# Performance work log

Measured on AMD Instinct MI355X. Metric: run time of the kernel, lower is better.

The kernel has to match this reference:

```python
import jax, jax.numpy as jnp
import numpy as np

CM = 8        # channel_mult
EPS = 1e-5    # BatchNorm eps
NEG = 0.2     # LeakyReLU slope


def conv2d(x, w, stride, pad, b=None):
    y = jax.lax.conv_general_dilated(
        x, w, (stride, stride), [(pad, pad), (pad, pad)],
        dimension_numbers=('NCHW', 'OIHW', 'NCHW'))
    if b is not None:
        y = y + b[None, :, None, None]
    return y


def per_sample_conv(x, w, stride, pad):
    # x: [B,C,H,W], w: [B,O,C,kh,kw] -> per-sample conv, vmapped over batch
    f = lambda xi, wi: conv2d(xi[None], wi, stride, pad)[0]
    return jax.vmap(f)(x, w)


def batchnorm(x, g, b):
    # training-mode BN: batch statistics over (N,H,W)
    m = jnp.mean(x, axis=(0, 2, 3), keepdims=True)
    v = jnp.var(x, axis=(0, 2, 3), keepdims=True)
    return (x - m) * jax.lax.rsqrt(v + EPS) * g[None, :, None, None] + b[None, :, None, None]


def lrelu(x):
    return jnp.where(x >= 0, x, NEG * x)


def setup_inputs() -> dict:
    key = jax.random.key(0)
    ks = jax.random.split(key, 16)
    B, H, W = 16, 512, 512

    def rn(k, shape, fan_in):
        return jax.random.normal(k, shape, jnp.float32) * np.float32(1.0 / np.sqrt(fan_in))

    inp = {}
    inp['x'] = jax.random.normal(ks[0], (B, 3, H, W), jnp.float32)
    n_meta = 3 * (CM // 2) * 25 + CM * (CM * 2 // 2) * 25  # 300 + 1600 = 1900
    inp['conv_weights'] = jax.random.normal(ks[1], (B, n_meta), jnp.float32) * 0.05
    inp['w11'] = rn(ks[2], (CM // 2, 3, 5, 5), 3 * 25)
    inp['b11'] = jnp.zeros((CM // 2,), jnp.float32)
    inp['w12'] = rn(ks[3], (CM * 2 // 2, CM, 5, 5), CM * 25)
    inp['b12'] = jnp.zeros((CM * 2 // 2,), jnp.float32)
    inp['bn1_g'] = jnp.ones((CM * 2,), jnp.float32)
    inp['bn1_b'] = jnp.zeros((CM * 2,), jnp.float32)
    # conv2 stack: (in, out, kernel)
    chans = [(CM * 2, CM * 4, 5), (CM * 4, CM * 8, 5), (CM * 8, CM * 16, 3), (CM * 16, CM * 16, 3)]
    for i, (ci, co, k) in enumerate(chans, 1):
        inp[f'c2w{i}'] = rn(ks[3 + i], (co, ci, k, k), ci * k * k)
        inp[f'c2b{i}'] = jnp.zeros((co,), jnp.float32)
        inp[f'bn{i}g'] = jnp.ones((co,), jnp.float32)
        inp[f'bn{i}b'] = jnp.zeros((co,), jnp.float32)
    return inp


def reference(x, conv_weights, w11, b11, w12, b12, bn1_g, bn1_b,
              c2w1, c2b1, bn1g, bn1b, c2w2, c2b2, bn2g, bn2b,
              c2w3, c2b3, bn3g, bn3b, c2w4, c2b4, bn4g, bn4b):
    B, _, H, W = x.shape
    n1 = 3 * (CM // 2) * 25
    w1 = conv_weights[:, :n1].reshape(B, CM // 2, 3, 5, 5)
    w2 = conv_weights[:, n1:].reshape(B, CM * 2 // 2, CM, 5, 5)

    # meta layer 1: shared half + per-sample dynamic half
    xx = conv2d(x, w11, 1, 2, b11)                  # [B, cm/2, H, W]
    half = per_sample_conv(x, w1, 1, 2)             # [B, cm/2, H, W]
    h = lrelu(jnp.concatenate([xx, half], axis=1))  # [B, cm, H, W]

    # meta layer 2 (stride 2)
    xx = conv2d(h, w12, 2, 2, b12)                  # [B, cm, H/2, W/2]
    half = per_sample_conv(h, w2, 2, 2)             # [B, cm, H/2, W/2]
    h = lrelu(batchnorm(jnp.concatenate([xx, half], axis=1), bn1_g, bn1_b))

    # dense conv stack
    for w_, b_, g_, be_, p in [
        (c2w1, c2b1, bn1g, bn1b, 2),
        (c2w2, c2b2, bn2g, bn2b, 2),
        (c2w3, c2b3, bn3g, bn3b, 1),
        (c2w4, c2b4, bn4g, bn4b, 1),
    ]:
        h = lrelu(batchnorm(conv2d(h, w_, 2, p, b_), g_, be_))

    return h.reshape(-1, CM * 16, H // 32, W // 32)
```

## Files before the change

kernel.cpp:

```cpp
#include <hip/hip_runtime.h>


typedef __attribute__((ext_vector_type(8))) short short8v;
typedef __attribute__((ext_vector_type(4))) float float4v;
typedef __attribute__((ext_vector_type(4))) unsigned short ushort4v;
typedef unsigned short u16;

#define LRELU_NEG 0.2f
#define BN_EPS 1e-5f

__device__ __forceinline__ float bf2f(u16 u){ union{unsigned i; float f;} v; v.i=(unsigned)u<<16; return v.f; }
__device__ __forceinline__ u16 f2bf(float f){ unsigned x=__float_as_uint(f); x += 0x7FFFu + ((x>>16)&1u); return (u16)(x>>16); }
__device__ __forceinline__ float lrelu(float v){ return v<0.f? LRELU_NEG*v : v; }

__device__ __forceinline__ void packw(int i, const float* __restrict__ w, u16* __restrict__ dst,
                                      int IC, int OC, int KSZ, int CPR) {
  int kq = i & 31, oc = (i>>5) % OC, c = i/(OC*32);
  int ky = c / CPR, r = c % CPR;
  int kk = r*32 + kq; int kx = kk / IC, ic = kk % IC;
  float v = (kx < KSZ) ? w[(((size_t)oc*IC + ic)*KSZ + ky)*KSZ + kx] : 0.f;
  dst[i] = f2bf(v);
}

__global__ __launch_bounds__(256) void prep_all(
    const float* __restrict__ w11, const float* __restrict__ w12,
    const float* __restrict__ b12, const float* __restrict__ cw,
    const float* __restrict__ wc1, const float* __restrict__ wc2,
    const float* __restrict__ wc3, const float* __restrict__ wc4,
    u16* __restrict__ wl1d, u16* __restrict__ wl2m, float* __restrict__ bl2,
    u16* __restrict__ d1, u16* __restrict__ d2, u16* __restrict__ d3, u16* __restrict__ d4,
    u16* __restrict__ h1) {
  int i = blockIdx.x*256 + threadIdx.x;
  if (i < 16) {
    bl2[i] = (i<8)? b12[i] : 0.f;
  } else if (i < 49168) {
    int j = i - 16;
    int b = j / 3072, r = j % 3072;
    int c = r >> 9, r2 = r & 511;
    int row = r2 >> 5, kk = r2 & 31;
    int kx = kk >> 2, ic = kk & 3;
    int grp = row >> 3, oc = row & 7;
    int ky = c - grp;
    float v = 0.f;
    if (ic < 3 && kx < 5 && ky >= 0 && ky < 5)
      v = (oc < 4) ? w11[((oc*3+ic)*5+ky)*5+kx]
                   : cw[b*1900 + (oc-4)*75 + ic*25 + ky*5 + kx];
    wl1d[j] = f2bf(v);
  } else if (i < 131088) {
    int j = i - 49168;
    int kq = j & 31, oc = (j>>5) & 15, c = (j>>9) % 10, b = j / 5120;
    int ky = c >> 1, r = c & 1;
    int kk = r*32 + kq; int kx = kk >> 3, ic = kk & 7;
    float v = 0.f;
    if (kx < 5)
      v = (oc < 8) ? w12[((oc*8+ic)*5+ky)*5+kx]
                   : cw[b*1900 + 300 + ((oc-8)*8+ic)*25 + ky*5 + kx];
    wl2m[j] = f2bf(v);
  } else if (i < 196880) {
    int j = i - 131088;
    int b = j / 4112, p = j % 4112;
    int y, xx;
    if (p < 2064) { int r = p/516; y = (r<2)? r : 512+r; xx = p%516; }
    else          { int q = p-2064; int cidx = q&3; xx = (cidx<2)? cidx : 512+cidx; y = 2 + (q>>2); }
    short8v z = {0,0,0,0,0,0,0,0};
    *(short8v*)(h1 + (((size_t)b*516 + y)*516 + xx)*8) = z;
  } else if (i < 484624) {
    int j = i - 196880;
    if (j < 15360) packw(j, wc1, d1, 16, 32, 5, 3);
    else if (j < 66560) packw(j-15360, wc2, d2, 32, 64, 5, 5);
    else if (j < 140288) packw(j-66560, wc3, d3, 64, 128, 3, 6);
    else packw(j-140288, wc4, d4, 128, 128, 3, 12);
  }
}

__global__ __launch_bounds__(256) void conv_l1(const float* __restrict__ x,
    const u16* __restrict__ wl1d, const float* __restrict__ b11,
    u16* __restrict__ h1) {
  __shared__ __align__(16) u16 sx[20*72*4 + 32];
  const int tid = threadIdx.x, b = blockIdx.z;
  const int x0 = (blockIdx.x & 7) * 64;
  const int r0 = (blockIdx.x >> 3) * 16;

  if (tid < 32) sx[20*72*4 + tid] = 0;

  const bool interior = (r0 >= 16) & (r0 <= 480) & (x0 >= 64) & (x0 <= 384);
  if (interior) {
    for (int e = tid; e < 360; e += 256) {
      int row = e / 18, cg = e % 18;
      size_t base = ((size_t)b*3*512 + r0 + row - 2)*512 + x0 + cg*4 - 4;
      float4v p0 = *(const float4v*)(x + base);
      float4v p1 = *(const float4v*)(x + base + 262144);
      float4v p2 = *(const float4v*)(x + base + 524288);
      short8v lo, hi;
#pragma unroll
      for (int j = 0; j < 2; j++) {
        lo[4*j+0] = (short)f2bf(p0[j]);   lo[4*j+1] = (short)f2bf(p1[j]);
        lo[4*j+2] = (short)f2bf(p2[j]);   lo[4*j+3] = 0;
        hi[4*j+0] = (short)f2bf(p0[j+2]); hi[4*j+1] = (short)f2bf(p1[j+2]);
        hi[4*j+2] = (short)f2bf(p2[j+2]); hi[4*j+3] = 0;
      }
      u16* dp = sx + (row*72 + cg*4)*4;
      *(short8v*)dp = lo;
      *(short8v*)(dp + 8) = hi;
    }
  } else {
    for (int e = tid; e < 1440; e += 256) {
      int row = e / 72, col = e % 72;
      int gy = r0 + row - 2, gx = x0 + col - 4;
      float v0 = 0.f, v1 = 0.f, v2 = 0.f;
      if (gy >= 0 && gy < 512 && gx >= 0 && gx < 512) {
        size_t base = ((size_t)b*3*512 + gy)*512 + gx;
        v0 = x[base]; v1 = x[base + 262144]; v2 = x[base + 524288];
      }
      ushort4 pk = {f2bf(v0), f2bf(v1), f2bf(v2), 0};
      *(ushort4*)(sx + e*4) = pk;
    }
  }
  __syncthreads();

  const int lane = tid & 63, w = tid >> 6;
  const int l15 = lane & 15, sub = lane >> 4;

  short8v Wf[6];
  const u16* wb = wl1d + (size_t)b*3072;
#pragma unroll
  for (int c = 0; c < 6; c++)
    Wf[c] = *(const short8v*)(wb + (c*16 + l15)*32 + sub*8);

  float bvv[4];
#pragma unroll
  for (int r = 0; r < 4; r++) bvv[r] = (sub & 1) ? 0.f : b11[r];

  const int colb = w*16 + l15;
  const int oc0 = (sub & 1) * 4;
  const int rsel = sub >> 1;

#pragma unroll
  for (int p = 0; p < 8; p++) {
    float4v acc = {0.f, 0.f, 0.f, 0.f};
#pragma unroll
    for (int c = 0; c < 6; c++) {
      const u16* ap = sx + (((2*p + c)*72 + colb + 2) << 2) + sub*8;
      union { unsigned long long q[2]; short8v v; } ua;
      ua.q[0] = *(const unsigned long long*)(ap);
      ua.q[1] = *(const unsigned long long*)(ap + 4);
      acc = __builtin_amdgcn_mfma_f32_16x16x32_bf16(Wf[c], ua.v, acc, 0, 0, 0);
    }
    ushort4v pk;
#pragma unroll
    for (int r = 0; r < 4; r++) pk[r] = f2bf(lrelu(acc[r] + bvv[r]));
    int outrow = r0 + 2*p + rsel;
    u16* dst = h1 + (((size_t)b*516 + outrow + 2)*516 + x0 + colb + 2)*8 + oc0;
    *(ushort4v*)dst = pk;
  }
}

#define LOADC(cc, Ax, Bx) do {                                                   \
    const int ky_ = (cc) / CPR, r_ = (cc) % CPR;                                 \
    const int kk0_ = r_*32 + sub*8;                                              \
    const int kx_ = kk0_ / IC, ico_ = kk0_ % IC;                                 \
    _Pragma("unroll") for (int n_ = 0; n_ < WN; n_++)                            \
      Bx[n_] = *(const short8v*)(wbase + ((size_t)(cc)*OC + oc0 + n_*16 + l15)*32 + sub*8); \
    _Pragma("unroll") for (int f_ = 0; f_ < WM; f_++) {                          \
      int iy_ = S*oyf[f_] + ky_ + PADOFF;                                        \
      Ax[f_] = *(const short8v*)(inb + ((size_t)iy_*IPW + ixb[f_] + kx_)*IC + ico_); \
    }                                                                            \
  } while(0)

#define MFMAC(Ax, Bx) do {                                                       \
    _Pragma("unroll") for (int f_ = 0; f_ < WM; f_++)                            \
      _Pragma("unroll") for (int n_ = 0; n_ < WN; n_++)                          \
        acc[f_][n_] = __builtin_amdgcn_mfma_f32_16x16x32_bf16(Ax[f_], Bx[n_], acc[f_][n_], 0, 0, 0); \
  } while(0)

template <int IC, int OC, int KSZ, int S, int P, int CPR, int NCH,
          int IPH, int IPW, int OWL, int OPH, int OPW,
          int WM, int WN, int WVM, int WVN, bool PERS>
__global__ __launch_bounds__(WVM*WVN*64) void conv_mfma(
    const u16* __restrict__ in, const u16* __restrict__ wmfma,
    const float* __restrict__ bias, u16* __restrict__ out,
    float2* __restrict__ part2) {
  constexpr int OW = 1 << OWL;
  constexpr int PADOFF = 2 - P;
  const int tid = threadIdx.x, lane = tid & 63;
  const int w = tid >> 6, wm = w % WVM, wn = w / WVM;
  const int l15 = lane & 15, sub = lane >> 4;
  const int b = blockIdx.z;
  const int px0 = blockIdx.x * (16*WM*WVM) + wm * (16*WM);
  const int oc0 = blockIdx.y * (16*WN*WVN) + wn * (16*WN);

  int oyf[WM], oxb[WM], ixb[WM];
#pragma unroll
  for (int f = 0; f < WM; f++) {
    int p = px0 + f*16;
    oyf[f] = p >> OWL;
    oxb[f] = p & (OW-1);
    ixb[f] = S*(oxb[f] + l15) + PADOFF;
  }
  const u16* inb = in + (size_t)b*IPH*IPW*IC;
  const u16* wbase = wmfma + (PERS ? (size_t)b*NCH*OC*32 : (size_t)0);

  float4v acc[WM][WN];
#pragma unroll
  for (int f = 0; f < WM; f++)
#pragma unroll
    for (int n = 0; n < WN; n++) acc[f][n] = (float4v){0.f,0.f,0.f,0.f};

  constexpr int NC = KSZ * CPR;
  short8v A0[WM], B0[WN], A1[WM], B1[WN];
  LOADC(0, A0, B0);
#pragma unroll
  for (int c = 0; c < NC; c += 2) {
    if (c + 1 < NC) LOADC(c + 1, A1, B1);
    MFMAC(A0, B0);
    if (c + 2 < NC) LOADC(c + 2, A0, B0);
    if (c + 1 < NC) MFMAC(A1, B1);
  }

  float s[WN], q[WN];
#pragma unroll
  for (int n = 0; n < WN; n++) { s[n] = 0.f; q[n] = 0.f; }
#pragma unroll
  for (int f = 0; f < WM; f++) {
    const int oxs = oxb[f] + sub*4;
    const size_t rowb = ((size_t)b*OPH + oyf[f] + 2)*OPW;
#pragma unroll
    for (int n = 0; n < WN; n++) {
      int oc = oc0 + n*16 + l15;
      float bv = bias[oc];
#pragma unroll
      for (int rr = 0; rr < 4; rr++) {
        float v = acc[f][n][rr] + bv;
        out[(rowb + oxs + rr + 2)*OC + oc] = f2bf(v);
        s[n] += v; q[n] += v*v;
      }
    }
  }
#pragma unroll
  for (int n = 0; n < WN; n++) {
    s[n] += __shfl_xor(s[n], 16); s[n] += __shfl_xor(s[n], 32);
    q[n] += __shfl_xor(q[n], 16); q[n] += __shfl_xor(q[n], 32);
  }
  __shared__ float sred[WVM*WVN][WN][16][2];
  if (sub == 0) {
#pragma unroll
    for (int n = 0; n < WN; n++) { sred[w][n][l15][0] = s[n]; sred[w][n][l15][1] = q[n]; }
  }
  __syncthreads();
  const int NBp = gridDim.x * gridDim.z;
  const int pb = blockIdx.z * gridDim.x + blockIdx.x;
  const int tot = WVN*WN*16;
  if (tid < tot) {
    int c16 = tid & 15, n = (tid >> 4) % WN, wn2 = tid / (16*WN);
    float S_ = 0.f, Q_ = 0.f;
    for (int wm2 = 0; wm2 < WVM; wm2++) {
      S_ += sred[wn2*WVM + wm2][n][c16][0];
      Q_ += sred[wn2*WVM + wm2][n][c16][1];
    }
    int c = blockIdx.y*(16*WN*WVN) + wn2*(16*WN) + n*16 + c16;
    part2[(size_t)c*NBp + pb] = make_float2(S_, Q_);
  }
}

__global__ void bn_stage2(const float2* __restrict__ part2, const float* __restrict__ g,
                          const float* __restrict__ bb, float* __restrict__ stats,
                          int NBp, float invN) {
  int c = blockIdx.x;
  float s = 0.f, q = 0.f;
  for (int i = threadIdx.x; i < NBp; i += 64) {
    float2 p = part2[(size_t)c*NBp + i];
    s += p.x; q += p.y;
  }
  for (int o = 32; o > 0; o >>= 1) { s += __shfl_down(s, o); q += __shfl_down(q, o); }
  if (threadIdx.x == 0) {
    float m = s * invN;
    float var = q * invN - m*m;
    float sc = g[c] * rsqrtf(var + BN_EPS);
    stats[2*c] = sc;
    stats[2*c+1] = bb[c] - m*sc;
  }
}

template <int C, int PH, int PW, int HH, int WW>
__global__ __launch_bounds__(256) void bn_fin(u16* __restrict__ y, const float* __restrict__ stats,
                                              int total8) {
  int i = blockIdx.x*256 + threadIdx.x;
  if (i >= total8) return;
  size_t e = (size_t)i*8;
  int c0 = (int)(e & (C-1));
  int px = (int)(e / C);
  int xx = px % PW;
  int yy = (px / PW) % PH;
  bool interior = (yy >= 2) & (yy < 2+HH) & (xx >= 2) & (xx < 2+WW);
  short8v u = *(short8v*)(y + e);
  short8v o;
#pragma unroll
  for (int j = 0; j < 8; j++) {
    float v = bf2f((u16)u[j]) * stats[2*(c0+j)] + stats[2*(c0+j)+1];
    o[j] = interior ? (short)f2bf(lrelu(v)) : (short)0;
  }
  *(short8v*)(y + e) = o;
}

__global__ __launch_bounds__(256) void out_k(const u16* __restrict__ y6,
                                             const float* __restrict__ stats,
                                             float* __restrict__ out) {
  int i = blockIdx.x*256 + threadIdx.x;
  if (i >= 131072) return;
  size_t e = (size_t)i*4;
  int c0 = (int)(e & 127);
  int px = (int)(e >> 7);
  int loc = px & 255, b = px >> 8;
  int y = loc >> 4, x = loc & 15;
  const u16* src = y6 + (((size_t)b*20 + y + 2)*20 + x + 2)*128 + c0;
  ushort4 u = *(const ushort4*)src;
  float vv[4] = {bf2f(u.x), bf2f(u.y), bf2f(u.z), bf2f(u.w)};
#pragma unroll
  for (int j = 0; j < 4; j++) {
    int c = c0 + j;
    float v = vv[j] * stats[2*c] + stats[2*c+1];
    out[(((size_t)b*128 + c) << 8) + loc] = lrelu(v);
  }
}

extern "C" void kernel_launch(void* const* d_in, const int* in_sizes, int n_in,
                              void* d_out, int out_size, void* d_ws, size_t ws_size,
                              hipStream_t stream) {
  const float* x    = (const float*)d_in[0];
  const float* cw   = (const float*)d_in[1];
  const float* w11  = (const float*)d_in[2];
  const float* b11  = (const float*)d_in[3];
  const float* w12  = (const float*)d_in[4];
  const float* b12  = (const float*)d_in[5];
  const float* bn1g = (const float*)d_in[6];
  const float* bn1b = (const float*)d_in[7];
  const float* c2w[4] = {(const float*)d_in[8], (const float*)d_in[12],
                         (const float*)d_in[16], (const float*)d_in[20]};
  const float* c2b[4] = {(const float*)d_in[9], (const float*)d_in[13],
                         (const float*)d_in[17], (const float*)d_in[21]};
  const float* bng[4] = {(const float*)d_in[10], (const float*)d_in[14],
                         (const float*)d_in[18], (const float*)d_in[22]};
  const float* bnb[4] = {(const float*)d_in[11], (const float*)d_in[15],
                         (const float*)d_in[19], (const float*)d_in[23]};

  char* ws = (char*)d_ws;
  u16* h1   = (u16*)(ws);
  u16* y3   = (u16*)(ws);
  u16* y4   = (u16*)(ws + 17842176);
  u16* y5   = (u16*)(ws + 27312128);
  u16* y6   = (u16*)(ws + 32620544);
  u16* yT2  = (u16*)(ws + 68158464);
  u16* wl2m = (u16*)(ws + 102769664);
  float* bl2    = (float*)(ws + 102933504);
  float2* part2 = (float2*)(ws + 102933568);
  float* stats2 = (float*)(ws + 103457856);
  float* stats3 = stats2 + 32;
  float* stats4 = stats3 + 64;
  float* stats5 = stats4 + 128;
  float* stats6 = stats5 + 256;
  u16* wl1d = (u16*)(ws + 103460800);
  u16* wS1  = (u16*)(ws + 103559104);
  u16* wS2  = (u16*)(ws + 103589824);
  u16* wS3  = (u16*)(ws + 103692224);
  u16* wS4  = (u16*)(ws + 103839680);

  prep_all<<<1894, 256, 0, stream>>>(w11, w12, b12, cw,
                                     c2w[0], c2w[1], c2w[2], c2w[3],
                                     wl1d, wl2m, bl2, wS1, wS2, wS3, wS4, h1);

  conv_l1<<<dim3(256, 1, 16), 256, 0, stream>>>(x, wl1d, b11, h1);

  conv_mfma<8,16,5,2,2, 2,10, 516,516, 8, 260,260, 4,1,4,1, true>
      <<<dim3(256,1,16), 256, 0, stream>>>(h1, wl2m, bl2, yT2, part2);

  bn_stage2<<<16, 64, 0, stream>>>(part2, bn1g, bn1b, stats2, 4096, 1.f/1048576.f);
  bn_fin<16,260,260,256,256><<<8450, 256, 0, stream>>>(yT2, stats2, 2163200);

  conv_mfma<16,32,5,2,2, 3,15, 260,260, 7, 132,132, 2,2,4,1, false>
      <<<dim3(128,1,16), 256, 0, stream>>>(yT2, wS1, c2b[0], y3, part2);
  bn_stage2<<<32, 64, 0, stream>>>(part2, bng[0], bnb[0], stats3, 2048, 1.f/262144.f);
  bn_fin<32,132,132,128,128><<<4356, 256, 0, stream>>>(y3, stats3, 1115136);

  conv_mfma<32,64,5,2,2, 5,25, 132,132, 6, 68,68, 2,2,2,2, false>
      <<<dim3(64,1,16), 256, 0, stream>>>(y3, wS2, c2b[1], y4, part2);
  bn_stage2<<<64, 64, 0, stream>>>(part2, bng[1], bnb[1], stats4, 1024, 1.f/65536.f);
  bn_fin<64,68,68,64,64><<<2312, 256, 0, stream>>>(y4, stats4, 591872);

  conv_mfma<64,128,3,2,1, 6,18, 68,68, 5, 36,36, 2,2,2,2, false>
      <<<dim3(16,2,16), 256, 0, stream>>>(y4, wS3, c2b[2], y5, part2);
  bn_stage2<<<128, 64, 0, stream>>>(part2, bng[2], bnb[2], stats5, 256, 1.f/16384.f);
  bn_fin<128,36,36,32,32><<<1296, 256, 0, stream>>>(y5, stats5, 331776);

  conv_mfma<128,128,3,2,1, 12,36, 36,36, 4, 20,20, 2,2,1,2, false>
      <<<dim3(8,2,16), 128, 0, stream>>>(y5, wS4, c2b[3], y6, part2);
  bn_stage2<<<128, 64, 0, stream>>>(part2, bng[3], bnb[3], stats6, 128, 1.f/4096.f);

  out_k<<<512, 256, 0, stream>>>(y6, stats6, (float*)d_out);
}
```

Measured before the change: 268.2 us.

## Store padded activations in even/odd column-split layout for stride-2 convs

Changes the padded NHWC activation layout so each row is split into even and odd column halves, and updates every producer and consumer (layer-1 writer, border zeroing, conv epilogue, bn_fin, out_k) to match. Stride-2 convolution loads then read consecutive columns within a parity half, so the 16 lanes of an MFMA fragment touch contiguous memory rather than every other pixel. This aims to improve coalescing and cache-line use of the A-operand loads. The index math is more complex, and the hardcoded stride of 2 assumes every conv_mfma instantiation is stride 2.

After: 252.6 us. 5.8% less time.

```diff
diff --git a/kernel.cpp b/kernel.cpp
--- a/kernel.cpp
+++ b/kernel.cpp
@@ -63,7 +63,7 @@
     if (p < 2064) { int r = p/516; y = (r<2)? r : 512+r; xx = p%516; }
     else          { int q = p-2064; int cidx = q&3; xx = (cidx<2)? cidx : 512+cidx; y = 2 + (q>>2); }
     short8v z = {0,0,0,0,0,0,0,0};
-    *(short8v*)(h1 + (((size_t)b*516 + y)*516 + xx)*8) = z;
+    *(short8v*)(h1 + ((((size_t)b*516 + y)*2 + (xx&1))*258 + (xx>>1))*8) = z;
   } else if (i < 484624) {
     int j = i - 196880;
     if (j < 15360) packw(j, wc1, d1, 16, 32, 5, 3);
@@ -134,6 +134,8 @@
   const int colb = w*16 + l15;
   const int oc0 = (sub & 1) * 4;
   const int rsel = sub >> 1;
+  const int x_out = x0 + colb + 2;
+  const int xpar = x_out & 1, xp = x_out >> 1;
 
 #pragma unroll
   for (int p = 0; p < 8; p++) {
@@ -150,7 +152,7 @@
 #pragma unroll
     for (int r = 0; r < 4; r++) pk[r] = f2bf(lrelu(acc[r] + bvv[r]));
     int outrow = r0 + 2*p + rsel;
-    u16* dst = h1 + (((size_t)b*516 + outrow + 2)*516 + x0 + colb + 2)*8 + oc0;
+    u16* dst = h1 + ((((size_t)b*516 + outrow + 2)*2 + xpar)*258 + xp)*8 + oc0;
     *(ushort4v*)dst = pk;
   }
 }
@@ -159,11 +161,12 @@
     const int ky_ = (cc) / CPR, r_ = (cc) % CPR;                                 \
     const int kk0_ = r_*32 + sub*8;                                              \
     const int kx_ = kk0_ / IC, ico_ = kk0_ % IC;                                 \
+    const int t_ = kx_ + PADOFF;                                                 \
     _Pragma("unroll") for (int n_ = 0; n_ < WN; n_++)                            \
       Bx[n_] = *(const short8v*)(wbase + ((size_t)(cc)*OC + oc0 + n_*16 + l15)*32 + sub*8); \
     _Pragma("unroll") for (int f_ = 0; f_ < WM; f_++) {                          \
-      int iy_ = S*oyf[f_] + ky_ + PADOFF;                                        \
-      Ax[f_] = *(const short8v*)(inb + ((size_t)iy_*IPW + ixb[f_] + kx_)*IC + ico_); \
+      int iy_ = 2*oyf[f_] + ky_ + PADOFF;                                        \
+      Ax[f_] = *(const short8v*)(inb + (((size_t)iy_*2 + (t_&1))*IPWH + axb[f_] + (t_>>1))*IC + ico_); \
     }                                                                            \
   } while(0)
 
@@ -182,6 +185,8 @@
     float2* __restrict__ part2) {
   constexpr int OW = 1 << OWL;
   constexpr int PADOFF = 2 - P;
+  constexpr int IPWH = IPW / 2;
+  constexpr int OPWH = OPW / 2;
   const int tid = threadIdx.x, lane = tid & 63;
   const int w = tid >> 6, wm = w % WVM, wn = w / WVM;
   const int l15 = lane & 15, sub = lane >> 4;
@@ -189,13 +194,13 @@
   const int px0 = blockIdx.x * (16*WM*WVM) + wm * (16*WM);
   const int oc0 = blockIdx.y * (16*WN*WVN) + wn * (16*WN);
 
-  int oyf[WM], oxb[WM], ixb[WM];
+  int oyf[WM], oxb[WM], axb[WM];
 #pragma unroll
   for (int f = 0; f < WM; f++) {
     int p = px0 + f*16;
     oyf[f] = p >> OWL;
     oxb[f] = p & (OW-1);
-    ixb[f] = S*(oxb[f] + l15) + PADOFF;
+    axb[f] = oxb[f] + l15;
   }
   const u16* inb = in + (size_t)b*IPH*IPW*IC;
   const u16* wbase = wmfma + (PERS ? (size_t)b*NCH*OC*32 : (size_t)0);
@@ -223,7 +228,7 @@
 #pragma unroll
   for (int f = 0; f < WM; f++) {
     const int oxs = oxb[f] + sub*4;
-    const size_t rowb = ((size_t)b*OPH + oyf[f] + 2)*OPW;
+    const size_t rowb2 = ((size_t)b*OPH + oyf[f] + 2)*2;
 #pragma unroll
     for (int n = 0; n < WN; n++) {
       int oc = oc0 + n*16 + l15;
@@ -231,7 +236,8 @@
 #pragma unroll
       for (int rr = 0; rr < 4; rr++) {
         float v = acc[f][n][rr] + bv;
-        out[(rowb + oxs + rr + 2)*OC + oc] = f2bf(v);
+        int x_out = oxs + rr + 2;
+        out[((rowb2 + (x_out & 1))*OPWH + (x_out >> 1))*OC + oc] = f2bf(v);
         s[n] += v; q[n] += v*v;
       }
     }
@@ -289,9 +295,10 @@
   size_t e = (size_t)i*8;
   int c0 = (int)(e & (C-1));
   int px = (int)(e / C);
-  int xx = px % PW;
-  int yy = (px / PW) % PH;
-  bool interior = (yy >= 2) & (yy < 2+HH) & (xx >= 2) & (xx < 2+WW);
+  int xp = px % (PW/2);
+  int t2 = px / (PW/2);
+  int yy = (t2 >> 1) % PH;
+  bool interior = (yy >= 2) & (yy < 2+HH) & (xp >= 1) & (xp <= WW/2);
   short8v u = *(short8v*)(y + e);
   short8v o;
 #pragma unroll
@@ -312,7 +319,8 @@
   int px = (int)(e >> 7);
   int loc = px & 255, b = px >> 8;
   int y = loc >> 4, x = loc & 15;
-  const u16* src = y6 + (((size_t)b*20 + y + 2)*20 + x + 2)*128 + c0;
+  int xi = x + 2;
+  const u16* src = y6 + ((((size_t)b*20 + y + 2)*2 + (xi & 1))*10 + (xi >> 1))*128 + c0;
   ushort4 u = *(const ushort4*)src;
   float vv[4] = {bf2f(u.x), bf2f(u.y), bf2f(u.z), bf2f(u.w)};
 #pragma unroll
```
